# Optimization experiments

Measured on AMD Instinct MI355X. Metric: run time of the kernel, lower is better.

Reference implementation:

```python
import jax, jax.numpy as jnp
import numpy as np

DIM = 1024
NUM_HEADS = 16
HEAD_DIM = 64
SEQ_LEN = 4096
RMS_EPS = 1e-6


def rotary_tables(T, head_dim):
    # modded-nanogpt style rotary: frequencies only on first half of the half-dim,
    # second half zeroed (identity rotation).
    angular_freq = (1.0 / 1024.0) ** jnp.linspace(0.0, 1.0, head_dim // 4)
    angular_freq = jnp.concatenate([angular_freq, jnp.zeros(head_dim // 4)])
    t = jnp.arange(T, dtype=jnp.float32)
    theta = t[:, None] * angular_freq[None, :]  # [T, D/2]
    return jnp.cos(theta), jnp.sin(theta)


def apply_rotary(x, cos, sin):
    # x: [B, T, H, D]
    xf = x.astype(jnp.float32)
    x1, x2 = jnp.split(xf, 2, axis=-1)
    c = cos[None, :, None, :]
    s = sin[None, :, None, :]
    y1 = x1 * c + x2 * s
    y2 = x1 * (-s) + x2 * c
    return jnp.concatenate([y1, y2], axis=-1).astype(x.dtype)


def rms_norm(x):
    return x * jax.lax.rsqrt(jnp.mean(x * x, axis=-1, keepdims=True) + RMS_EPS)


def setup_inputs() -> dict:
    key = jax.random.key(0)
    k1, k2, k3 = jax.random.split(key, 3)
    hdim = NUM_HEADS * HEAD_DIM
    std = 0.5 * DIM ** (-0.5)
    bound = (3.0 ** 0.5) * std
    x = jax.random.normal(k1, (1, SEQ_LEN, DIM), dtype=jnp.float32)
    qkv_w = jax.random.uniform(k2, (3 * hdim, DIM), minval=-bound, maxval=bound, dtype=jnp.float32)
    # original zero-inits c_proj; use small random weights for a nontrivial baseline
    proj_w = jax.random.normal(k3, (DIM, hdim), dtype=jnp.float32) * 0.02
    lambdas = jnp.array([0.5], dtype=jnp.float32)
    return {"x": x, "qkv_w": qkv_w, "lambdas": lambdas, "proj_w": proj_w}


def reference(x, qkv_w, lambdas, proj_w):
    B, T, _ = x.shape
    H, D = NUM_HEADS, HEAD_DIM
    scale = 1.0 / (D ** 0.5)
    qkv = jnp.einsum('btc,fc->btf', x, qkv_w)            # [B, T, 3*H*D]
    qkv = qkv.reshape(B, T, 3 * H, D)
    q, k, v = jnp.split(qkv, 3, axis=-2)                  # each [B, T, H, D]
    q, k = rms_norm(q), rms_norm(k)
    cos, sin = rotary_tables(T, D)
    q, k = apply_rotary(q, cos, sin), apply_rotary(k, cos, sin)
    v = lambdas[0] * v
    scores = jnp.einsum('bqhd,bkhd->bhqk', q, k) * scale  # [B, H, T, T]
    causal = jnp.tril(jnp.ones((T, T), dtype=bool))
    scores = jnp.where(causal[None, None], scores, -jnp.inf)
    p = jax.nn.softmax(scores, axis=-1)
    y = jnp.einsum('bhqk,bkhd->bqhd', p, v)               # [B, T, H, D]
    y = y.reshape(B, T, H * D)
    return jnp.einsum('btf,cf->btc', y, proj_w)           # [B, T, DIM]
```

## Files before the change

kernel.cpp:

```cpp
#include <hip/hip_runtime.h>
#include <stdint.h>

#define SEQ 4096
#define NHEAD 16
#define HDIM 64

typedef __attribute__((ext_vector_type(4))) float f32x4;
typedef __attribute__((ext_vector_type(16))) float f32x16;
typedef __attribute__((ext_vector_type(8))) __bf16 bf16x8;
typedef __attribute__((ext_vector_type(8))) unsigned short u16x8;
typedef __attribute__((ext_vector_type(4))) unsigned short u16x4;
typedef __attribute__((ext_vector_type(4))) unsigned int u32x4;

static __device__ __forceinline__ float bf2f(unsigned short u) {
    unsigned int x = ((unsigned int)u) << 16;
    return __builtin_bit_cast(float, x);
}
static __device__ __forceinline__ unsigned short f2bf(float f) {
    unsigned int u = __builtin_bit_cast(unsigned int, f);
    u += 0x7FFFu + ((u >> 16) & 1u);
    return (unsigned short)(u >> 16);
}
static __device__ __forceinline__ f32x4 mfma_bf16_16x16x32(u16x8 a, u16x8 b, f32x4 c) {
    return __builtin_amdgcn_mfma_f32_16x16x32_bf16(
        __builtin_bit_cast(bf16x8, a), __builtin_bit_cast(bf16x8, b), c, 0, 0, 0);
}
static __device__ __forceinline__ f32x16 mfma_bf16_32x32x16(u16x8 a, u16x8 b, f32x16 c) {
    return __builtin_amdgcn_mfma_f32_32x32x16_bf16(
        __builtin_bit_cast(bf16x8, a), __builtin_bit_cast(bf16x8, b), c, 0, 0, 0);
}
static __device__ __forceinline__ void gload_lds16(const void* g, void* l) {
    __builtin_amdgcn_global_load_lds(
        (__attribute__((address_space(1))) unsigned int*)g,
        (__attribute__((address_space(3))) unsigned int*)l,
        16, 0, 0);
}
static __device__ __forceinline__ unsigned int cvtpk_bf16(float lo, float hi) {
    unsigned int r;
    asm("v_cvt_pk_bf16_f32 %0, %1, %2" : "=v"(r) : "v"(lo), "v"(hi));
    return r;
}

__global__ void cvt3_kernel(const float* __restrict__ s0, unsigned short* __restrict__ d0, int n0q,
                            const float* __restrict__ s1, unsigned short* __restrict__ d1, int n1q,
                            const float* __restrict__ s2, unsigned short* __restrict__ d2, int n2q)
{
    const int stride = gridDim.x * blockDim.x;
    const int total = n0q + n1q + n2q;
    for (int i = blockIdx.x * blockDim.x + threadIdx.x; i < total; i += stride) {
        const float* src; unsigned short* dst; int j;
        if (i < n0q)            { src = s0; dst = d0; j = i; }
        else if (i < n0q + n1q) { src = s1; dst = d1; j = i - n0q; }
        else                    { src = s2; dst = d2; j = i - n0q - n1q; }
        f32x4 v = *(const f32x4*)(src + (size_t)j * 4);
        u16x4 o;
#pragma unroll
        for (int k = 0; k < 4; k++) o[k] = f2bf(v[k]);
        *(u16x4*)(dst + (size_t)j * 4) = o;
    }
}

template<int OUT_BF16>
__global__ __launch_bounds__(256) void gemm_bt_kernel(
    const unsigned short* __restrict__ A,
    const unsigned short* __restrict__ B,
    void* __restrict__ Cv,
    int M, int N, int K, int lda)
{
    __shared__ __align__(16) unsigned short As[128 * 64];
    __shared__ __align__(16) unsigned short Bs[128 * 64];
    const int tid = threadIdx.x;
    const int lane = tid & 63;
    const int wave = tid >> 6;
    const int wm = (wave >> 1) * 64;
    const int wn = (wave & 1) * 64;
    const int bm = blockIdx.y * 128, bn = blockIdx.x * 128;
    const int l15 = lane & 15, l4 = lane >> 4;

    f32x4 acc[4][4];
#pragma unroll
    for (int i = 0; i < 4; i++)
#pragma unroll
        for (int j = 0; j < 4; j++) acc[i][j] = (f32x4){0.f, 0.f, 0.f, 0.f};

    const int srow = tid >> 3;
    const int scol = (tid & 7) * 8;
    const unsigned short* Ab = A + (size_t)(bm + srow) * lda + scol;
    const unsigned short* Bb = B + (size_t)(bn + srow) * K + scol;

    for (int kt = 0; kt < K; kt += 64) {
#pragma unroll
        for (int ci = 0; ci < 4; ci++)
            gload_lds16(Ab + (size_t)ci * 32 * lda + kt, &As[ci * 2048 + tid * 8]);
#pragma unroll
        for (int ci = 0; ci < 4; ci++)
            gload_lds16(Bb + (size_t)ci * 32 * K + kt, &Bs[ci * 2048 + tid * 8]);
        __syncthreads();
#pragma unroll
        for (int ks = 0; ks < 2; ks++) {
            const int kc = ks * 32 + l4 * 8;
            u16x8 af[4], bfr[4];
#pragma unroll
            for (int i = 0; i < 4; i++)
                af[i] = *(const u16x8*)&As[(wm + i * 16 + l15) * 64 + kc];
#pragma unroll
            for (int j = 0; j < 4; j++)
                bfr[j] = *(const u16x8*)&Bs[(wn + j * 16 + l15) * 64 + kc];
#pragma unroll
            for (int i = 0; i < 4; i++)
#pragma unroll
                for (int j = 0; j < 4; j++)
                    acc[i][j] = mfma_bf16_16x16x32(af[i], bfr[j], acc[i][j]);
        }
        __syncthreads();
    }

    const int orow = bm + wm + l4 * 4;
    const int ocol = bn + wn + l15;
#pragma unroll
    for (int i = 0; i < 4; i++)
#pragma unroll
        for (int j = 0; j < 4; j++)
#pragma unroll
            for (int r = 0; r < 4; r++) {
                size_t idx = (size_t)(orow + i * 16 + r) * N + (ocol + j * 16);
                if (OUT_BF16) ((unsigned short*)Cv)[idx] = f2bf(acc[i][j][r]);
                else          ((float*)Cv)[idx] = acc[i][j][r];
            }
}

__global__ __launch_bounds__(256) void rope_norm_kernel(
    const unsigned short* __restrict__ qkv,
    const float* __restrict__ lambdas,
    unsigned short* __restrict__ qh,
    unsigned short* __restrict__ kh,
    unsigned short* __restrict__ vh)
{
    const int lane = threadIdx.x & 63;
    const int wave = threadIdx.x >> 6;
    const int vec = blockIdx.x * 4 + wave;
    const int t = vec >> 4;
    const int h = vec & 15;
    const size_t base = (size_t)t * 3072 + h * 64 + lane;
    float q = bf2f(qkv[base]);
    float k = bf2f(qkv[base + 1024]);
    float v = bf2f(qkv[base + 2048]);
    float sq = q * q, sk = k * k;
#pragma unroll
    for (int m = 1; m < 64; m <<= 1) {
        sq += __shfl_xor(sq, m);
        sk += __shfl_xor(sk, m);
    }
    q *= rsqrtf(sq * (1.0f / 64.0f) + 1e-6f);
    k *= rsqrtf(sk * (1.0f / 64.0f) + 1e-6f);
    const int i = lane & 31;
    float w = (i < 16) ? exp2f(-(10.0f / 15.0f) * (float)i) : 0.0f;
    float th = (float)t * w;
    float c = cosf(th), s = sinf(th);
    float qp = __shfl_xor(q, 32);
    float kp = __shfl_xor(k, 32);
    float sg = (lane < 32) ? s : -s;
    float qo = (q * c + qp * sg) * 0.1803368801111244f;
    float ko = k * c + kp * sg;
    float vo = v * lambdas[0];
    const size_t o = ((size_t)h * SEQ + t) * 64 + lane;
    qh[o] = f2bf(qo);
    kh[o] = f2bf(ko);
    vh[o] = f2bf(vo);
}

__global__ __launch_bounds__(256) void transpose_v_kernel(
    const unsigned short* __restrict__ vh, unsigned short* __restrict__ vT)
{
    __shared__ __align__(16) unsigned short tile[64][72];
    const int h = blockIdx.x >> 6;
    const int tt = (blockIdx.x & 63) * 64;
    const int tid = threadIdx.x;
    const int row = tid >> 2;
    const int c0 = (tid & 3) * 16;
    const u16x8* src = (const u16x8*)(vh + ((size_t)h * SEQ + tt + row) * 64 + c0);
    u16x8 a = src[0], b = src[1];
#pragma unroll
    for (int j = 0; j < 8; j++) { tile[row][c0 + j] = a[j]; tile[row][c0 + 8 + j] = b[j]; }
    __syncthreads();
    u16x8 o0, o1;
#pragma unroll
    for (int j = 0; j < 8; j++) { o0[j] = tile[c0 + j][row]; o1[j] = tile[c0 + 8 + j][row]; }
    u16x8* dst = (u16x8*)(vT + ((size_t)h * 64 + row) * SEQ + tt + c0);
    dst[0] = o0; dst[1] = o1;
}

__global__ __launch_bounds__(256, 3) void attn_kernel(
    const unsigned short* __restrict__ qh,
    const unsigned short* __restrict__ kh,
    const unsigned short* __restrict__ vT,
    float* __restrict__ acc,
    float* __restrict__ lacc)
{
    __shared__ __align__(16) unsigned short Ks[2][64 * 64];
    __shared__ __align__(16) unsigned short Vs[2][64 * 64];
    const int h = blockIdx.x;
    const int qp = blockIdx.y;
    const int s = blockIdx.z;
    const int tid = threadIdx.x;
    const int lane = tid & 63;
    const int wave = tid >> 6;
    const int l31 = lane & 31;
    const int hi = lane >> 5;
    const int r7 = l31 & 7;

    const unsigned short* Kb = kh + (size_t)h * SEQ * 64;
    const unsigned short* Vb = vT + (size_t)h * 64 * SEQ;

    const int sr = tid >> 3;
    const int scs = ((tid & 7) * 8) ^ ((sr & 7) * 8);

#pragma unroll 1
    for (int ph = 0; ph < 2; ph++) {
        const int qtp = ph ? (31 - qp) : qp;
        const int nt = 2 * qtp + 2;
        const int t0 = (nt * s) / 3;
        const int t1 = (nt * (s + 1)) / 3;
        if (t0 >= t1) continue;
        const int q0w = qtp * 128 + wave * 32;

        u16x8 qf[4];
        {
            const unsigned short* qb = qh + ((size_t)h * SEQ + q0w + l31) * 64 + hi * 8;
#pragma unroll
            for (int c = 0; c < 4; c++) qf[c] = *(const u16x8*)(qb + c * 16);
        }

        f32x16 o0 = {}, o1 = {};
        float l = 0.f;

        const unsigned short* kst = Kb + (size_t)(t0 * 64 + sr) * 64 + scs;
        const unsigned short* vst = Vb + (size_t)sr * SEQ + t0 * 64 + scs;

        gload_lds16(kst,            &Ks[0][tid * 8]);
        gload_lds16(kst + 32 * 64,  &Ks[0][2048 + tid * 8]);
        gload_lds16(vst,            &Vs[0][tid * 8]);
        gload_lds16(vst + 32 * SEQ, &Vs[0][2048 + tid * 8]);
        kst += 64 * 64;
        vst += 64;
        __syncthreads();

        int cur = 0;
        for (int kt = t0; kt < t1; kt++) {
            const int kv0 = kt * 64;
            if (kt + 1 < t1) {
                gload_lds16(kst,            &Ks[cur ^ 1][tid * 8]);
                gload_lds16(kst + 32 * 64,  &Ks[cur ^ 1][2048 + tid * 8]);
                gload_lds16(vst,            &Vs[cur ^ 1][tid * 8]);
                gload_lds16(vst + 32 * SEQ, &Vs[cur ^ 1][2048 + tid * 8]);
            }
            kst += 64 * 64;
            vst += 64;
            if (kv0 <= q0w + 31) {
                const unsigned short* ks0 = &Ks[cur][l31 * 64];
                const unsigned short* vs0 = &Vs[cur][l31 * 64];
                const unsigned short* ks1 = ks0 + 32 * 64;
                const unsigned short* vs1 = vs0 + 32 * 64;
                const bool half2 = (kv0 + 32 <= q0w + 31);
                const int q = q0w + l31;
                float ts;

                {
                    f32x16 st = {};
                    __builtin_amdgcn_s_setprio(1);
#pragma unroll
                    for (int c = 0; c < 4; c++) {
                        const int off = ((c * 2 + hi) ^ r7) * 8;
                        st = mfma_bf16_32x32x16(*(const u16x8*)(ks0 + off), qf[c], st);
                    }
                    __builtin_amdgcn_s_setprio(0);
                    if (kv0 + 31 > q0w) {
#pragma unroll
                        for (int r = 0; r < 16; r++) {
                            const int crow = (r & 3) + 8 * (r >> 2) + 4 * hi;
                            if (kv0 + crow > q) st[r] = -1e30f;
                        }
                    }
#pragma unroll
                    for (int r = 0; r < 16; r++) st[r] = exp2f(st[r]);
                    float u8[8];
#pragma unroll
                    for (int r = 0; r < 8; r++) u8[r] = st[r] + st[r + 8];
#pragma unroll
                    for (int r = 0; r < 4; r++) u8[r] += u8[r + 4];
                    ts = (u8[0] + u8[2]) + (u8[1] + u8[3]);

                    u16x8 paf[2];
#pragma unroll
                    for (int kk = 0; kk < 2; kk++) {
                        const int rb = kk * 8;
                        unsigned int a0 = cvtpk_bf16(st[rb + 0], st[rb + 1]);
                        unsigned int a1 = cvtpk_bf16(st[rb + 2], st[rb + 3]);
                        unsigned int b0 = cvtpk_bf16(st[rb + 4], st[rb + 5]);
                        unsigned int b1 = cvtpk_bf16(st[rb + 6], st[rb + 7]);
                        asm volatile("v_permlane32_swap_b32 %0, %1" : "+v"(a0), "+v"(b0));
                        asm volatile("v_permlane32_swap_b32 %0, %1" : "+v"(a1), "+v"(b1));
                        u32x4 w;
                        w[0] = a0; w[1] = a1; w[2] = b0; w[3] = b1;
                        paf[kk] = __builtin_bit_cast(u16x8, w);
                    }
                    __builtin_amdgcn_s_setprio(1);
#pragma unroll
                    for (int kk = 0; kk < 2; kk++) {
                        const int off = ((kk * 2 + hi) ^ r7) * 8;
                        u16x8 v0 = *(const u16x8*)(vs0 + off);
                        u16x8 v1 = *(const u16x8*)(vs1 + off);
                        o0 = mfma_bf16_32x32x16(paf[kk], v0, o0);
                        o1 = mfma_bf16_32x32x16(paf[kk], v1, o1);
                    }
                    __builtin_amdgcn_s_setprio(0);
                }

                if (half2) {
                    f32x16 st = {};
                    __builtin_amdgcn_s_setprio(1);
#pragma unroll
                    for (int c = 0; c < 4; c++) {
                        const int off = ((c * 2 + hi) ^ r7) * 8;
                        st = mfma_bf16_32x32x16(*(const u16x8*)(ks1 + off), qf[c], st);
                    }
                    __builtin_amdgcn_s_setprio(0);
                    if (kv0 + 63 > q0w) {
#pragma unroll
                        for (int r = 0; r < 16; r++) {
                            const int crow = (r & 3) + 8 * (r >> 2) + 4 * hi;
                            if (kv0 + 32 + crow > q) st[r] = -1e30f;
                        }
                    }
#pragma unroll
                    for (int r = 0; r < 16; r++) st[r] = exp2f(st[r]);
                    float u8[8];
#pragma unroll
                    for (int r = 0; r < 8; r++) u8[r] = st[r] + st[r + 8];
#pragma unroll
                    for (int r = 0; r < 4; r++) u8[r] += u8[r + 4];
                    ts += (u8[0] + u8[2]) + (u8[1] + u8[3]);

                    u16x8 paf[2];
#pragma unroll
                    for (int kk = 0; kk < 2; kk++) {
                        const int rb = kk * 8;
                        unsigned int a0 = cvtpk_bf16(st[rb + 0], st[rb + 1]);
                        unsigned int a1 = cvtpk_bf16(st[rb + 2], st[rb + 3]);
                        unsigned int b0 = cvtpk_bf16(st[rb + 4], st[rb + 5]);
                        unsigned int b1 = cvtpk_bf16(st[rb + 6], st[rb + 7]);
                        asm volatile("v_permlane32_swap_b32 %0, %1" : "+v"(a0), "+v"(b0));
                        asm volatile("v_permlane32_swap_b32 %0, %1" : "+v"(a1), "+v"(b1));
                        u32x4 w;
                        w[0] = a0; w[1] = a1; w[2] = b0; w[3] = b1;
                        paf[kk] = __builtin_bit_cast(u16x8, w);
                    }
                    __builtin_amdgcn_s_setprio(1);
#pragma unroll
                    for (int kk = 0; kk < 2; kk++) {
                        const int off = (((kk + 2) * 2 + hi) ^ r7) * 8;
                        u16x8 v0 = *(const u16x8*)(vs0 + off);
                        u16x8 v1 = *(const u16x8*)(vs1 + off);
                        o0 = mfma_bf16_32x32x16(paf[kk], v0, o0);
                        o1 = mfma_bf16_32x32x16(paf[kk], v1, o1);
                    }
                    __builtin_amdgcn_s_setprio(0);
                }

                ts += __shfl_xor(ts, 32);
                l += ts;
            }
            __syncthreads();
            cur ^= 1;
        }

        if (t0 * 64 <= q0w + 31) {
#pragma unroll
            for (int r = 0; r < 16; r++) {
                const int crow = (r & 3) + 8 * (r >> 2) + 4 * hi;
                float* row = acc + (size_t)(q0w + crow) * 1024 + h * 64;
                atomicAdd(row + l31,      o0[r]);
                atomicAdd(row + 32 + l31, o1[r]);
            }
            if (hi == 0) atomicAdd(lacc + (size_t)(q0w + l31) * 16 + h, l);
        }
    }
}

__global__ __launch_bounds__(256) void norm_kernel(
    const float* __restrict__ acc, const float* __restrict__ lacc,
    unsigned short* __restrict__ yb)
{
    const int i = blockIdx.x * 256 + threadIdx.x;
    const int t = i >> 8;
    const int h = (i & 255) >> 4;
    const float inv = 1.0f / lacc[t * 16 + h];
    f32x4 v = *(const f32x4*)(acc + (size_t)i * 4);
    u16x4 o;
#pragma unroll
    for (int j = 0; j < 4; j++) o[j] = f2bf(v[j] * inv);
    *(u16x4*)(yb + (size_t)i * 4) = o;
}

extern "C" void kernel_launch(void* const* d_in, const int* in_sizes, int n_in,
                              void* d_out, int out_size, void* d_ws, size_t ws_size,
                              hipStream_t stream) {
    (void)in_sizes; (void)n_in; (void)out_size; (void)ws_size;
    const float* x       = (const float*)d_in[0];
    const float* qkv_w   = (const float*)d_in[1];
    const float* lambdas = (const float*)d_in[2];
    const float* proj_w  = (const float*)d_in[3];

    char* ws = (char*)d_ws;
    unsigned short* x_bf   = (unsigned short*)(ws + 0);
    unsigned short* qkv_bf = (unsigned short*)(ws + 8388608);
    unsigned short* qh     = (unsigned short*)(ws + 33554432);
    unsigned short* kh     = (unsigned short*)(ws + 41943040);
    unsigned short* vh     = (unsigned short*)(ws + 50331648);
    unsigned short* vT     = (unsigned short*)(ws + 58720256);
    unsigned short* wq_bf  = (unsigned short*)(ws + 67108864);
    unsigned short* wp_bf  = (unsigned short*)(ws + 73400320);
    unsigned short* yb     = (unsigned short*)(ws + 75497472);
    float*          acc    = (float*)(ws + 0);
    float*          lacc   = (float*)(ws + 16777216);

    cvt3_kernel<<<2048, 256, 0, stream>>>(x, x_bf, 1048576,
                                          qkv_w, wq_bf, 786432,
                                          proj_w, wp_bf, 262144);

    gemm_bt_kernel<1><<<dim3(24, 32), 256, 0, stream>>>(x_bf, wq_bf, qkv_bf, 4096, 3072, 1024, 1024);
    rope_norm_kernel<<<16384, 256, 0, stream>>>(qkv_bf, lambdas, qh, kh, vh);
    transpose_v_kernel<<<1024, 256, 0, stream>>>(vh, vT);

    hipMemsetAsync(ws, 0, 16777216 + 262144, stream);

    attn_kernel<<<dim3(16, 16, 3), 256, 0, stream>>>(qh, kh, vT, acc, lacc);
    norm_kernel<<<4096, 256, 0, stream>>>(acc, lacc, yb);

    gemm_bt_kernel<0><<<dim3(8, 32), 256, 0, stream>>>(yb, wp_bf, d_out, 4096, 1024, 1024, 1024);
}
```

Before: 190.8 us.

## Fuse rope/norm with V transpose, compute row sums via MFMA, split KV in two

Merges the rope/RMS-norm kernel and the V transpose kernel into one, so V goes through shared memory directly and the intermediate vh buffer write and read disappear. In attention, the softmax row sum is now computed with an extra MFMA against a ones vector instead of scalar adds and a cross-lane shuffle. The KV split drops from three to two (grid z), and launch bounds drop to two blocks per CU. The risks are fewer atomics in flight, lower occupancy and load balance, and extra MFMA work for the row-sum accumulation.

After: 194.1 us. About the same (+1.7%).

```diff
diff --git a/kernel.cpp b/kernel.cpp
--- a/kernel.cpp
+++ b/kernel.cpp
@@ -129,60 +129,54 @@
             }
 }
 
-__global__ __launch_bounds__(256) void rope_norm_kernel(
+__global__ __launch_bounds__(256) void rope_norm_tr_kernel(
     const unsigned short* __restrict__ qkv,
     const float* __restrict__ lambdas,
     unsigned short* __restrict__ qh,
     unsigned short* __restrict__ kh,
-    unsigned short* __restrict__ vh)
-{
-    const int lane = threadIdx.x & 63;
-    const int wave = threadIdx.x >> 6;
-    const int vec = blockIdx.x * 4 + wave;
-    const int t = vec >> 4;
-    const int h = vec & 15;
-    const size_t base = (size_t)t * 3072 + h * 64 + lane;
-    float q = bf2f(qkv[base]);
-    float k = bf2f(qkv[base + 1024]);
-    float v = bf2f(qkv[base + 2048]);
-    float sq = q * q, sk = k * k;
-#pragma unroll
-    for (int m = 1; m < 64; m <<= 1) {
-        sq += __shfl_xor(sq, m);
-        sk += __shfl_xor(sk, m);
-    }
-    q *= rsqrtf(sq * (1.0f / 64.0f) + 1e-6f);
-    k *= rsqrtf(sk * (1.0f / 64.0f) + 1e-6f);
-    const int i = lane & 31;
-    float w = (i < 16) ? exp2f(-(10.0f / 15.0f) * (float)i) : 0.0f;
-    float th = (float)t * w;
-    float c = cosf(th), s = sinf(th);
-    float qp = __shfl_xor(q, 32);
-    float kp = __shfl_xor(k, 32);
-    float sg = (lane < 32) ? s : -s;
-    float qo = (q * c + qp * sg) * 0.1803368801111244f;
-    float ko = k * c + kp * sg;
-    float vo = v * lambdas[0];
-    const size_t o = ((size_t)h * SEQ + t) * 64 + lane;
-    qh[o] = f2bf(qo);
-    kh[o] = f2bf(ko);
-    vh[o] = f2bf(vo);
-}
-
-__global__ __launch_bounds__(256) void transpose_v_kernel(
-    const unsigned short* __restrict__ vh, unsigned short* __restrict__ vT)
+    unsigned short* __restrict__ vT)
 {
     __shared__ __align__(16) unsigned short tile[64][72];
     const int h = blockIdx.x >> 6;
     const int tt = (blockIdx.x & 63) * 64;
+    const int lane = threadIdx.x & 63;
+    const int wave = threadIdx.x >> 6;
+    const float lam = lambdas[0];
+    const int i = lane & 31;
+    const float w = (i < 16) ? exp2f(-(10.0f / 15.0f) * (float)i) : 0.0f;
+
+#pragma unroll 1
+    for (int it = 0; it < 16; it++) {
+        const int tl = it * 4 + wave;
+        const int t = tt + tl;
+        const size_t base = (size_t)t * 3072 + h * 64 + lane;
+        float q = bf2f(qkv[base]);
+        float k = bf2f(qkv[base + 1024]);
+        float v = bf2f(qkv[base + 2048]);
+        float sq = q * q, sk = k * k;
+#pragma unroll
+        for (int m = 1; m < 64; m <<= 1) {
+            sq += __shfl_xor(sq, m);
+            sk += __shfl_xor(sk, m);
+        }
+        q *= rsqrtf(sq * (1.0f / 64.0f) + 1e-6f);
+        k *= rsqrtf(sk * (1.0f / 64.0f) + 1e-6f);
+        float th = (float)t * w;
+        float c = cosf(th), s = sinf(th);
+        float qp = __shfl_xor(q, 32);
+        float kp = __shfl_xor(k, 32);
+        float sg = (lane < 32) ? s : -s;
+        float qo = (q * c + qp * sg) * 0.1803368801111244f;
+        float ko = k * c + kp * sg;
+        const size_t o = ((size_t)h * SEQ + t) * 64 + lane;
+        qh[o] = f2bf(qo);
+        kh[o] = f2bf(ko);
+        tile[tl][lane] = f2bf(v * lam);
+    }
+    __syncthreads();
     const int tid = threadIdx.x;
     const int row = tid >> 2;
     const int c0 = (tid & 3) * 16;
-    const u16x8* src = (const u16x8*)(vh + ((size_t)h * SEQ + tt + row) * 64 + c0);
-    u16x8 a = src[0], b = src[1];
-#pragma unroll
-    for (int j = 0; j < 8; j++) { tile[row][c0 + j] = a[j]; tile[row][c0 + 8 + j] = b[j]; }
-    __syncthreads();
     u16x8 o0, o1;
 #pragma unroll
     for (int j = 0; j < 8; j++) { o0[j] = tile[c0 + j][row]; o1[j] = tile[c0 + 8 + j][row]; }
@@ -190,7 +184,7 @@
     dst[0] = o0; dst[1] = o1;
 }
 
-__global__ __launch_bounds__(256, 3) void attn_kernel(
+__global__ __launch_bounds__(256, 2) void attn_kernel(
     const unsigned short* __restrict__ qh,
     const unsigned short* __restrict__ kh,
     const unsigned short* __restrict__ vT,
@@ -212,6 +206,10 @@
     const unsigned short* Kb = kh + (size_t)h * SEQ * 64;
     const unsigned short* Vb = vT + (size_t)h * 64 * SEQ;
 
+    u16x8 ones;
+#pragma unroll
+    for (int j = 0; j < 8; j++) ones[j] = 0x3F80;
+
     const int sr = tid >> 3;
     const int scs = ((tid & 7) * 8) ^ ((sr & 7) * 8);
 
@@ -219,9 +217,8 @@
     for (int ph = 0; ph < 2; ph++) {
         const int qtp = ph ? (31 - qp) : qp;
         const int nt = 2 * qtp + 2;
-        const int t0 = (nt * s) / 3;
-        const int t1 = (nt * (s + 1)) / 3;
-        if (t0 >= t1) continue;
+        const int t0 = (nt * s) >> 1;
+        const int t1 = (nt * (s + 1)) >> 1;
         const int q0w = qtp * 128 + wave * 32;
 
         u16x8 qf[4];
@@ -231,8 +228,7 @@
             for (int c = 0; c < 4; c++) qf[c] = *(const u16x8*)(qb + c * 16);
         }
 
-        f32x16 o0 = {}, o1 = {};
-        float l = 0.f;
+        f32x16 o0 = {}, o1 = {}, lA = {};
 
         const unsigned short* kst = Kb + (size_t)(t0 * 64 + sr) * 64 + scs;
         const unsigned short* vst = Vb + (size_t)sr * SEQ + t0 * 64 + scs;
@@ -263,7 +259,6 @@
                 const unsigned short* vs1 = vs0 + 32 * 64;
                 const bool half2 = (kv0 + 32 <= q0w + 31);
                 const int q = q0w + l31;
-                float ts;
 
                 {
                     f32x16 st = {};
@@ -283,12 +278,6 @@
                     }
 #pragma unroll
                     for (int r = 0; r < 16; r++) st[r] = exp2f(st[r]);
-                    float u8[8];
-#pragma unroll
-                    for (int r = 0; r < 8; r++) u8[r] = st[r] + st[r + 8];
-#pragma unroll
-                    for (int r = 0; r < 4; r++) u8[r] += u8[r + 4];
-                    ts = (u8[0] + u8[2]) + (u8[1] + u8[3]);
 
                     u16x8 paf[2];
 #pragma unroll
@@ -312,6 +301,7 @@
                         u16x8 v1 = *(const u16x8*)(vs1 + off);
                         o0 = mfma_bf16_32x32x16(paf[kk], v0, o0);
                         o1 = mfma_bf16_32x32x16(paf[kk], v1, o1);
+                        lA = mfma_bf16_32x32x16(paf[kk], ones, lA);
                     }
                     __builtin_amdgcn_s_setprio(0);
                 }
@@ -334,12 +324,6 @@
                     }
 #pragma unroll
                     for (int r = 0; r < 16; r++) st[r] = exp2f(st[r]);
-                    float u8[8];
-#pragma unroll
-                    for (int r = 0; r < 8; r++) u8[r] = st[r] + st[r + 8];
-#pragma unroll
-                    for (int r = 0; r < 4; r++) u8[r] += u8[r + 4];
-                    ts += (u8[0] + u8[2]) + (u8[1] + u8[3]);
 
                     u16x8 paf[2];
 #pragma unroll
@@ -363,12 +347,10 @@
                         u16x8 v1 = *(const u16x8*)(vs1 + off);
                         o0 = mfma_bf16_32x32x16(paf[kk], v0, o0);
                         o1 = mfma_bf16_32x32x16(paf[kk], v1, o1);
+                        lA = mfma_bf16_32x32x16(paf[kk], ones, lA);
                     }
                     __builtin_amdgcn_s_setprio(0);
                 }
-
-                ts += __shfl_xor(ts, 32);
-                l += ts;
             }
             __syncthreads();
             cur ^= 1;
@@ -382,7 +364,13 @@
                 atomicAdd(row + l31,      o0[r]);
                 atomicAdd(row + 32 + l31, o1[r]);
             }
-            if (hi == 0) atomicAdd(lacc + (size_t)(q0w + l31) * 16 + h, l);
+            if (l31 == 0) {
+#pragma unroll
+                for (int r = 0; r < 16; r++) {
+                    const int crow = (r & 3) + 8 * (r >> 2) + 4 * hi;
+                    atomicAdd(lacc + (size_t)(q0w + crow) * 16 + h, lA[r]);
+                }
+            }
         }
     }
 }
@@ -416,7 +404,6 @@
     unsigned short* qkv_bf = (unsigned short*)(ws + 8388608);
     unsigned short* qh     = (unsigned short*)(ws + 33554432);
     unsigned short* kh     = (unsigned short*)(ws + 41943040);
-    unsigned short* vh     = (unsigned short*)(ws + 50331648);
     unsigned short* vT     = (unsigned short*)(ws + 58720256);
     unsigned short* wq_bf  = (unsigned short*)(ws + 67108864);
     unsigned short* wp_bf  = (unsigned short*)(ws + 73400320);
@@ -429,12 +416,11 @@
                                           proj_w, wp_bf, 262144);
 
     gemm_bt_kernel<1><<<dim3(24, 32), 256, 0, stream>>>(x_bf, wq_bf, qkv_bf, 4096, 3072, 1024, 1024);
-    rope_norm_kernel<<<16384, 256, 0, stream>>>(qkv_bf, lambdas, qh, kh, vh);
-    transpose_v_kernel<<<1024, 256, 0, stream>>>(vh, vT);
+    rope_norm_tr_kernel<<<1024, 256, 0, stream>>>(qkv_bf, lambdas, qh, kh, vT);
 
     hipMemsetAsync(ws, 0, 16777216 + 262144, stream);
 
-    attn_kernel<<<dim3(16, 16, 3), 256, 0, stream>>>(qh, kh, vT, acc, lacc);
+    attn_kernel<<<dim3(16, 16, 2), 256, 0, stream>>>(qh, kh, vT, acc, lacc);
     norm_kernel<<<4096, 256, 0, stream>>>(acc, lacc, yb);
 
     gemm_bt_kernel<0><<<dim3(8, 32), 256, 0, stream>>>(yb, wp_bf, d_out, 4096, 1024, 1024, 1024);
```
